# Optimization experiments

Hardware: AMD Instinct MI355X
Metric: run time of the kernel (lower is better)

## Reference

```python
import jax, jax.numpy as jnp
import numpy as np

B, T, D_IN, H, NUM_CLASSES = 1024, 512, 4, 64, 3
G = 4 * H  # gates: i, f, g, o (PyTorch order)


def setup_inputs() -> dict:
    key = jax.random.key(0)
    ks = jax.random.split(key, 32)
    s = 0.1  # small init scale, like PyTorch's 1/sqrt(H) uniform
    inp = {"x": jax.random.normal(ks[0], (B, T, D_IN), jnp.float32)}
    i = 1
    for l in range(4):
        d = D_IN if l == 0 else H
        inp[f"w_ih_{l}"] = s * jax.random.normal(ks[i], (G, d), jnp.float32); i += 1
        inp[f"w_hh_{l}"] = s * jax.random.normal(ks[i], (G, H), jnp.float32); i += 1
        inp[f"b_ih_{l}"] = s * jax.random.normal(ks[i], (G,), jnp.float32); i += 1
        inp[f"b_hh_{l}"] = s * jax.random.normal(ks[i], (G,), jnp.float32); i += 1
    inp["fc1_w"] = s * jax.random.normal(ks[i], (H // 2, H), jnp.float32); i += 1
    inp["fc1_b"] = s * jax.random.normal(ks[i], (H // 2,), jnp.float32); i += 1
    inp["fc2_w"] = s * jax.random.normal(ks[i], (NUM_CLASSES, H // 2), jnp.float32); i += 1
    inp["fc2_b"] = s * jax.random.normal(ks[i], (NUM_CLASSES,), jnp.float32)
    return inp


def _lstm_layer(x, w_ih, w_hh, b_ih, b_hh):
    # x: [B, T, d_in] -> [B, T, H]; PyTorch gate order i, f, g, o.
    b, t, _ = x.shape
    # Precompute input contribution for all timesteps in one GEMM.
    pre = jnp.einsum('btd,gd->tbg', x, w_ih) + (b_ih + b_hh)  # [T, B, 4H]
    h0 = jnp.zeros((b, H), x.dtype)
    c0 = jnp.zeros((b, H), x.dtype)

    def step(carry, p):
        h, c = carry
        gates = p + h @ w_hh.T  # [B, 4H]
        i_g, f_g, g_g, o_g = jnp.split(gates, 4, axis=-1)
        i_g = jax.nn.sigmoid(i_g)
        f_g = jax.nn.sigmoid(f_g)
        g_g = jnp.tanh(g_g)
        o_g = jax.nn.sigmoid(o_g)
        c = f_g * c + i_g * g_g
        h = o_g * jnp.tanh(c)
        return (h, c), h

    _, hs = jax.lax.scan(step, (h0, c0), pre)  # hs: [T, B, H]
    return hs.transpose(1, 0, 2)


def reference(x,
              w_ih_0, w_hh_0, b_ih_0, b_hh_0,
              w_ih_1, w_hh_1, b_ih_1, b_hh_1,
              w_ih_2, w_hh_2, b_ih_2, b_hh_2,
              w_ih_3, w_hh_3, b_ih_3, b_hh_3,
              fc1_w, fc1_b, fc2_w, fc2_b):
    layers = [(w_ih_0, w_hh_0, b_ih_0, b_hh_0),
              (w_ih_1, w_hh_1, b_ih_1, b_hh_1),
              (w_ih_2, w_hh_2, b_ih_2, b_hh_2),
              (w_ih_3, w_hh_3, b_ih_3, b_hh_3)]
    h = x
    for (wi, wh, bi, bh) in layers:
        h = _lstm_layer(h, wi, wh, bi, bh)
    last = h[:, -1, :]                         # [B, H]
    z = jax.nn.relu(last @ fc1_w.T + fc1_b)    # [B, H//2]
    logits = z @ fc2_w.T + fc2_b               # [B, 3]
    return jax.nn.softmax(logits, axis=1)
```

## Files before the change

kernel.cpp:

```cpp
#include <hip/hip_runtime.h>


#define TLEN 512
#define NCH  64

typedef __bf16 bf16x8 __attribute__((ext_vector_type(8)));
typedef float  f32x4  __attribute__((ext_vector_type(4)));

struct Params {
  const float* x;
  const float* wih[4]; const float* whh[4];
  const float* bih[4]; const float* bhh[4];
  const float* fc1w; const float* fc1b;
  const float* fc2w; const float* fc2b;
  float* out;
};

__device__ __forceinline__ bf16x8 bfzero() {
  union { unsigned long long u[2]; bf16x8 v; } z; z.u[0] = 0ull; z.u[1] = 0ull; return z.v;
}
__device__ __forceinline__ float fast_sigmoid(float x) {
  return __builtin_amdgcn_rcpf(1.f + __expf(-x));
}
__device__ __forceinline__ float fast_tanh(float x) {
  float e = __expf(2.f * x);
  return 1.f - 2.f * __builtin_amdgcn_rcpf(e + 1.f);
}

__global__ __launch_bounds__(1024) void lstm_fused(Params p)
{
  const int chunk = blockIdx.x;
  const int b0   = chunk * 16;
  const int tid  = threadIdx.x;
  const int wave = tid >> 6;
  const int L    = wave >> 2;
  const int w    = wave & 3;
  const int lane = tid & 63;
  const int quad = lane >> 4;
  const int l15  = lane & 15;

  __shared__ __bf16 tiles[2][5][16 * 64];
  __shared__ float  s_fc1w[2048];
  __shared__ float  s_z[512];
  __shared__ float  s_fc1b[32];
  __shared__ float  s_fc2w[96];
  __shared__ float  s_fc2b[3];

  bf16x8 wf[4][4];
  float  bias[4];
  {
    const float* wih = p.wih[L];
    const float* whh = p.whh[L];
    const float* bih = p.bih[L];
    const float* bhh = p.bhh[L];
#pragma unroll
    for (int g = 0; g < 4; g++) {
      int n = g * 64 + w * 16 + l15;
      bias[g] = bih[n] + bhh[n];
      if (L == 0) {
        bf16x8 f = bfzero();
        if (quad == 0) {
#pragma unroll
          for (int j = 0; j < 4; j++) f[j] = (__bf16)wih[n * 4 + j];
        }
        wf[g][0] = f; wf[g][1] = bfzero();
      } else {
#pragma unroll
        for (int q = 0; q < 2; q++) {
          const float* s = wih + n * 64 + q * 32 + quad * 8;
          bf16x8 f;
#pragma unroll
          for (int j = 0; j < 8; j++) f[j] = (__bf16)s[j];
          wf[g][q] = f;
        }
      }
#pragma unroll
      for (int q = 0; q < 2; q++) {
        const float* s = whh + n * 64 + q * 32 + quad * 8;
        bf16x8 f;
#pragma unroll
        for (int j = 0; j < 8; j++) f[j] = (__bf16)s[j];
        wf[g][2 + q] = f;
      }
    }
  }

  {
    int* ti = (int*)tiles;
    for (int i = tid; i < 5120; i += 1024) ti[i] = 0;
  }
  float cst[4] = {0.f, 0.f, 0.f, 0.f};

  if (wave == 0 && quad == 0) {
    const float4 xv = *(const float4*)(p.x + ((size_t)(b0 + l15) * TLEN) * 4);
    __bf16 v[4] = {(__bf16)xv.x, (__bf16)xv.y, (__bf16)xv.z, (__bf16)xv.w};
    *(float2*)&tiles[0][0][l15 * 64 + (l15 & 7) * 8] = *(float2*)v;
  }
  __syncthreads();

  for (int s = 0; s < TLEN + 3; s++) {
    const int t  = s - L;
    const int pr = s & 1;
    const int pw = pr ^ 1;

    if ((unsigned)t < (unsigned)TLEN) {
      const __bf16* in  = tiles[pr][L];
      const __bf16* own = tiles[pr][L + 1];
      const int sg0 = quad ^ (l15 & 7);
      const int sg1 = (4 + quad) ^ (l15 & 7);
      bf16x8 xf0 = *(const bf16x8*)&in [l15 * 64 + sg0 * 8];
      bf16x8 xf1 = *(const bf16x8*)&in [l15 * 64 + sg1 * 8];
      bf16x8 hf0 = *(const bf16x8*)&own[l15 * 64 + sg0 * 8];
      bf16x8 hf1 = *(const bf16x8*)&own[l15 * 64 + sg1 * 8];

      f32x4 acc[4];
#pragma unroll
      for (int g = 0; g < 4; g++) { f32x4 a = {bias[g], bias[g], bias[g], bias[g]}; acc[g] = a; }
#pragma unroll
      for (int g = 0; g < 4; g++) {
        acc[g] = __builtin_amdgcn_mfma_f32_16x16x32_bf16(xf0, wf[g][0], acc[g], 0, 0, 0);
        acc[g] = __builtin_amdgcn_mfma_f32_16x16x32_bf16(xf1, wf[g][1], acc[g], 0, 0, 0);
        acc[g] = __builtin_amdgcn_mfma_f32_16x16x32_bf16(hf0, wf[g][2], acc[g], 0, 0, 0);
        acc[g] = __builtin_amdgcn_mfma_f32_16x16x32_bf16(hf1, wf[g][3], acc[g], 0, 0, 0);
      }

      if (wave == 0 && quad == 0 && t + 1 < TLEN) {
        const float4 xv = *(const float4*)(p.x + ((size_t)(b0 + l15) * TLEN + (t + 1)) * 4);
        __bf16 v[4] = {(__bf16)xv.x, (__bf16)xv.y, (__bf16)xv.z, (__bf16)xv.w};
        *(float2*)&tiles[pw][0][l15 * 64 + (l15 & 7) * 8] = *(float2*)v;
      }

      const int col = w * 16 + l15;
      __bf16* dst = tiles[pw][L + 1];
#pragma unroll
      for (int r = 0; r < 4; r++) {
        float ig = fast_sigmoid(acc[0][r]);
        float fg = fast_sigmoid(acc[1][r]);
        float gg = fast_tanh(acc[2][r]);
        float og = fast_sigmoid(acc[3][r]);
        float c = fg * cst[r] + ig * gg;
        cst[r] = c;
        float h = og * fast_tanh(c);
        int m  = quad * 4 + r;
        int sg = (col >> 3) ^ (m & 7);
        dst[m * 64 + sg * 8 + (col & 7)] = (__bf16)h;
      }
    }

    __syncthreads();
  }

  for (int i = tid; i < 2048; i += 1024) s_fc1w[i] = p.fc1w[i];
  if (tid < 32) s_fc1b[tid] = p.fc1b[tid];
  if (tid < 96) s_fc2w[tid] = p.fc2w[tid];
  if (tid < 3)  s_fc2b[tid] = p.fc2b[tid];
  __syncthreads();
  if (tid < 512) {
    int m = tid >> 5, u = tid & 31;
    float sacc = s_fc1b[u];
    const float* wrow = &s_fc1w[u * 64];
    const __bf16* hfin = tiles[1][4];
#pragma unroll
    for (int k = 0; k < 64; k++) {
      int sg = (k >> 3) ^ (m & 7);
      sacc += (float)hfin[m * 64 + sg * 8 + (k & 7)] * wrow[k];
    }
    s_z[m * 32 + u] = fmaxf(sacc, 0.f);
  }
  __syncthreads();
  if (tid < 16) {
    int m = tid;
    float lg[3];
#pragma unroll
    for (int v = 0; v < 3; v++) {
      float sv = s_fc2b[v];
#pragma unroll
      for (int u = 0; u < 32; u++) sv += s_z[m * 32 + u] * s_fc2w[v * 32 + u];
      lg[v] = sv;
    }
    float mx = fmaxf(lg[0], fmaxf(lg[1], lg[2]));
    float e0 = __expf(lg[0] - mx), e1 = __expf(lg[1] - mx), e2 = __expf(lg[2] - mx);
    float inv = 1.f / (e0 + e1 + e2);
    float* o = p.out + (size_t)(b0 + m) * 3;
    o[0] = e0 * inv; o[1] = e1 * inv; o[2] = e2 * inv;
  }
}

extern "C" void kernel_launch(void* const* d_in, const int* in_sizes, int n_in,
                              void* d_out, int out_size, void* d_ws, size_t ws_size,
                              hipStream_t stream)
{
  (void)in_sizes; (void)n_in; (void)out_size; (void)d_ws; (void)ws_size;
  Params p;
  p.x = (const float*)d_in[0];
  for (int l = 0; l < 4; l++) {
    p.wih[l] = (const float*)d_in[1 + 4 * l];
    p.whh[l] = (const float*)d_in[2 + 4 * l];
    p.bih[l] = (const float*)d_in[3 + 4 * l];
    p.bhh[l] = (const float*)d_in[4 + 4 * l];
  }
  p.fc1w = (const float*)d_in[17];
  p.fc1b = (const float*)d_in[18];
  p.fc2w = (const float*)d_in[19];
  p.fc2b = (const float*)d_in[20];
  p.out = (float*)d_out;

  hipLaunchKernelGGL(lstm_fused, dim3(NCH), dim3(1024), 0, stream, p);
}
```

Before: 924.2 us.

## Split LSTM layers across two workgroups per chunk with a global-memory ring handoff

Adds a new kernel that runs layers 0-1 and layers 2-3 of each batch chunk in separate 512-thread workgroups (128 blocks total). The first workgroup streams its layer-1 hidden states to the second through a ring buffer in workspace memory, coordinated by atomic flag and ack counters with spin-waits. This spreads the work over twice as many CUs and shortens each block's pipeline skew and barrier cost. In exchange it adds cross-CU synchronisation latency on every step and needs both blocks of a chunk to be co-resident, otherwise the spin loops run until their cap. The old fused kernel remains as a fallback when the workspace is too small.

```diff
diff --git a/kernel.cpp b/kernel.cpp
--- a/kernel.cpp
+++ b/kernel.cpp
@@ -3,6 +3,8 @@
 
 #define TLEN 512
 #define NCH  64
+#define AG   __HIP_MEMORY_SCOPE_AGENT
+#define SPIN_CAP 500000
 
 typedef __bf16 bf16x8 __attribute__((ext_vector_type(8)));
 typedef float  f32x4  __attribute__((ext_vector_type(4)));
@@ -13,7 +15,8 @@
   const float* bih[4]; const float* bhh[4];
   const float* fc1w; const float* fc1b;
   const float* fc2w; const float* fc2b;
-  float* out;
+  float* out; char* ws;
+  int R; int Rmask; int D;
 };
 
 __device__ __forceinline__ bf16x8 bfzero() {
@@ -25,6 +28,279 @@
 __device__ __forceinline__ float fast_tanh(float x) {
   float e = __expf(2.f * x);
   return 1.f - 2.f * __builtin_amdgcn_rcpf(e + 1.f);
+}
+__device__ __forceinline__ void load_frag_pair(const unsigned short* sb, int l15, int quad,
+                                               bf16x8& f0, bf16x8& f1) {
+  const unsigned long long* a = (const unsigned long long*)(sb + l15 * 64 + quad * 8);
+  const unsigned long long* b = (const unsigned long long*)(sb + l15 * 64 + 32 + quad * 8);
+  union { bf16x8 v; unsigned long long u[2]; } c0, c1;
+  c0.u[0] = __hip_atomic_load(&a[0], __ATOMIC_RELAXED, AG);
+  c0.u[1] = __hip_atomic_load(&a[1], __ATOMIC_RELAXED, AG);
+  c1.u[0] = __hip_atomic_load(&b[0], __ATOMIC_RELAXED, AG);
+  c1.u[1] = __hip_atomic_load(&b[1], __ATOMIC_RELAXED, AG);
+  f0 = c0.v; f1 = c1.v;
+}
+
+__global__ __launch_bounds__(512, 2) void lstm_split(Params p)
+{
+  const int bid   = blockIdx.x;
+  const int role  = bid >> 6;
+  const int chunk = bid & 63;
+  const int b0    = chunk * 16;
+  const int tid   = threadIdx.x;
+  const int wave  = tid >> 6;
+  const int grp   = wave >> 2;
+  const int w     = wave & 3;
+  const int lane  = tid & 63;
+  const int quad  = lane >> 4;
+  const int l15   = lane & 15;
+  const int L     = role * 2 + grp;
+
+  __shared__ __bf16 tiles[2][2][1024];
+  __shared__ float  s_fc1w[2048];
+  __shared__ float  s_z[512];
+  __shared__ float  s_fc1b[32];
+  __shared__ float  s_fc2w[96];
+  __shared__ float  s_fc2b[3];
+
+  int* flagp = (int*)p.ws + chunk * 16;
+  int* ackp  = (int*)(p.ws + 16 * 1024) + chunk * 16;
+  unsigned short* ringc = (unsigned short*)(p.ws + 32 * 1024) + (size_t)chunk * p.R * 1024;
+  const int RM = p.Rmask;
+
+  bf16x8 wf[4][4];
+  float  bias[4];
+  {
+    const float* wih = p.wih[L];
+    const float* whh = p.whh[L];
+    const float* bih = p.bih[L];
+    const float* bhh = p.bhh[L];
+#pragma unroll
+    for (int g = 0; g < 4; g++) {
+      int n = g * 64 + w * 16 + l15;
+      bias[g] = bih[n] + bhh[n];
+      if (L == 0) {
+        bf16x8 f = bfzero();
+        if (quad == 0) {
+#pragma unroll
+          for (int j = 0; j < 4; j++) f[j] = (__bf16)wih[n * 4 + j];
+        }
+        wf[g][0] = f; wf[g][1] = bfzero();
+      } else {
+#pragma unroll
+        for (int q = 0; q < 2; q++) {
+          const float* s = wih + n * 64 + q * 32 + quad * 8;
+          bf16x8 f;
+#pragma unroll
+          for (int j = 0; j < 8; j++) f[j] = (__bf16)s[j];
+          wf[g][q] = f;
+        }
+      }
+#pragma unroll
+      for (int q = 0; q < 2; q++) {
+        const float* s = whh + n * 64 + q * 32 + quad * 8;
+        bf16x8 f;
+#pragma unroll
+        for (int j = 0; j < 8; j++) f[j] = (__bf16)s[j];
+        wf[g][2 + q] = f;
+      }
+    }
+  }
+
+  { int* ti = (int*)tiles; for (int i = tid; i < 2048; i += 512) ti[i] = 0; }
+  float cst[4] = {0.f, 0.f, 0.f, 0.f};
+
+  int W = 0, f_pend = 0;
+  int ackW = -1000000000, a_pend = -1000000000;
+  bf16x8 xA0 = bfzero(), xA1 = bfzero();
+
+  if (role == 0) {
+    if (grp == 0 && quad == 0) {
+      const float4 xv = *(const float4*)(p.x + ((size_t)(b0 + l15) * TLEN) * 4);
+      bf16x8 f = bfzero();
+      f[0] = (__bf16)xv.x; f[1] = (__bf16)xv.y; f[2] = (__bf16)xv.z; f[3] = (__bf16)xv.w;
+      xA0 = f;
+    }
+  } else if (grp == 0) {
+    const int G = (p.D > 2) ? p.D : 2;
+    int v = 0, it = 0;
+    do {
+      if (lane == 0) v = __hip_atomic_load(flagp, __ATOMIC_ACQUIRE, AG);
+      v = __shfl(v, 0);
+      if (v >= G) break;
+      __builtin_amdgcn_s_sleep(2);
+    } while (++it < SPIN_CAP);
+    W = v;
+    load_frag_pair(ringc, l15, quad, xA0, xA1);
+  }
+  __syncthreads();
+
+  for (int s = 0; s < TLEN + 1; s++) {
+    const int t  = s - grp;
+    const int pr = s & 1, pw = pr ^ 1;
+    bf16x8 xN0 = xA0, xN1 = xA1;
+
+    if ((unsigned)t < (unsigned)TLEN) {
+      bf16x8 if0, if1;
+      if (grp == 0) { if0 = xA0; if1 = xA1; }
+      else {
+        const __bf16* src = tiles[pr][0];
+        int sg0 = quad ^ (l15 & 7);
+        int sg1 = (4 + quad) ^ (l15 & 7);
+        if0 = *(const bf16x8*)&src[l15 * 64 + sg0 * 8];
+        if1 = *(const bf16x8*)&src[l15 * 64 + sg1 * 8];
+      }
+      bf16x8 hf0, hf1;
+      {
+        const __bf16* src = tiles[pr][grp];
+        int sg0 = quad ^ (l15 & 7);
+        int sg1 = (4 + quad) ^ (l15 & 7);
+        hf0 = *(const bf16x8*)&src[l15 * 64 + sg0 * 8];
+        hf1 = *(const bf16x8*)&src[l15 * 64 + sg1 * 8];
+      }
+
+      f32x4 acc[4];
+#pragma unroll
+      for (int g = 0; g < 4; g++) { f32x4 a = {bias[g], bias[g], bias[g], bias[g]}; acc[g] = a; }
+      if (L == 0) {
+#pragma unroll
+        for (int g = 0; g < 4; g++)
+          acc[g] = __builtin_amdgcn_mfma_f32_16x16x32_bf16(if0, wf[g][0], acc[g], 0, 0, 0);
+      } else {
+#pragma unroll
+        for (int g = 0; g < 4; g++) {
+          acc[g] = __builtin_amdgcn_mfma_f32_16x16x32_bf16(if0, wf[g][0], acc[g], 0, 0, 0);
+          acc[g] = __builtin_amdgcn_mfma_f32_16x16x32_bf16(if1, wf[g][1], acc[g], 0, 0, 0);
+        }
+      }
+#pragma unroll
+      for (int g = 0; g < 4; g++) {
+        acc[g] = __builtin_amdgcn_mfma_f32_16x16x32_bf16(hf0, wf[g][2], acc[g], 0, 0, 0);
+        acc[g] = __builtin_amdgcn_mfma_f32_16x16x32_bf16(hf1, wf[g][3], acc[g], 0, 0, 0);
+      }
+
+      if (role == 0 && grp == 0 && quad == 0 && t + 1 < TLEN) {
+        const float4 xv = *(const float4*)(p.x + ((size_t)(b0 + l15) * TLEN + (t + 1)) * 4);
+        bf16x8 f = bfzero();
+        f[0] = (__bf16)xv.x; f[1] = (__bf16)xv.y; f[2] = (__bf16)xv.z; f[3] = (__bf16)xv.w;
+        xN0 = f;
+      }
+      if (role == 0 && grp == 1 && t >= p.R && ackW < t + 1 - p.R) {
+        int v = ackW, it = 0;
+        do {
+          if (lane == 0) v = __hip_atomic_load(ackp, __ATOMIC_ACQUIRE, AG);
+          v = __shfl(v, 0);
+          if (v >= t + 1 - p.R) break;
+          __builtin_amdgcn_s_sleep(2);
+        } while (++it < SPIN_CAP);
+        ackW = v;
+      }
+
+      const int col = w * 16 + l15;
+      __bf16* dst = tiles[pw][grp];
+      unsigned hb[4];
+#pragma unroll
+      for (int r = 0; r < 4; r++) {
+        float ig = fast_sigmoid(acc[0][r]);
+        float fg = fast_sigmoid(acc[1][r]);
+        float gg = fast_tanh(acc[2][r]);
+        float og = fast_sigmoid(acc[3][r]);
+        float c = fg * cst[r] + ig * gg;
+        cst[r] = c;
+        float h = og * fast_tanh(c);
+        __bf16 hbf = (__bf16)h;
+        union { __bf16 b; unsigned short s; } cv; cv.b = hbf;
+        hb[r] = cv.s;
+        int m  = quad * 4 + r;
+        int sg = (col >> 3) ^ (m & 7);
+        dst[m * 64 + sg * 8 + (col & 7)] = hbf;
+      }
+      if (role == 0 && grp == 1) {
+        unsigned* rdst = (unsigned*)(ringc + (size_t)(t & RM) * 1024);
+#pragma unroll
+        for (int r = 0; r < 4; r++) {
+          unsigned v = hb[r];
+          unsigned o = (unsigned)__shfl_xor((int)v, 1);
+          if ((lane & 1) == 0) {
+            int m = quad * 4 + r;
+            __hip_atomic_store(&rdst[(m * 64 + col) >> 1], v | (o << 16), __ATOMIC_RELAXED, AG);
+          }
+        }
+      }
+    }
+
+    __syncthreads();
+
+    if (role == 0) {
+      if (tid == 0 && s >= 1)
+        __hip_atomic_store(flagp, s, __ATOMIC_RELAXED, AG);
+      if (grp == 1) {
+        int am = __shfl(a_pend, 0);
+        if (am > ackW) ackW = am;
+        if (lane == 0) a_pend = __hip_atomic_load(ackp, __ATOMIC_RELAXED, AG);
+      }
+    } else {
+      if (grp == 0) {
+        int fm = __shfl(f_pend, 0);
+        if (fm > W) W = fm;
+        if (lane == 0) f_pend = __hip_atomic_load(flagp, __ATOMIC_ACQUIRE, AG);
+        const int c = s;
+        if (c + 1 < TLEN) {
+          if (W < c + 2) {
+            int v = W, it = 0;
+            do {
+              if (lane == 0) v = __hip_atomic_load(flagp, __ATOMIC_ACQUIRE, AG);
+              v = __shfl(v, 0);
+              if (v >= c + 2) break;
+              __builtin_amdgcn_s_sleep(2);
+            } while (++it < SPIN_CAP);
+            W = v;
+          }
+          load_frag_pair(ringc + (size_t)((c + 1) & RM) * 1024, l15, quad, xN0, xN1);
+        }
+      }
+      if (tid == 0)
+        __hip_atomic_store(ackp, s, __ATOMIC_RELAXED, AG);
+    }
+    xA0 = xN0; xA1 = xN1;
+  }
+
+  if (role == 1) {
+    for (int i = tid; i < 2048; i += 512) s_fc1w[i] = p.fc1w[i];
+    if (tid < 32) s_fc1b[tid] = p.fc1b[tid];
+    if (tid < 96) s_fc2w[tid] = p.fc2w[tid];
+    if (tid < 3)  s_fc2b[tid] = p.fc2b[tid];
+    __syncthreads();
+    {
+      int m = tid >> 5, u = tid & 31;
+      float sacc = s_fc1b[u];
+      const float* wrow = &s_fc1w[u * 64];
+      const __bf16* hfin = tiles[1][1];
+#pragma unroll
+      for (int k = 0; k < 64; k++) {
+        int sg = (k >> 3) ^ (m & 7);
+        sacc += (float)hfin[m * 64 + sg * 8 + (k & 7)] * wrow[k];
+      }
+      s_z[m * 32 + u] = fmaxf(sacc, 0.f);
+    }
+    __syncthreads();
+    if (tid < 16) {
+      int m = tid;
+      float lg[3];
+#pragma unroll
+      for (int v = 0; v < 3; v++) {
+        float sv = s_fc2b[v];
+#pragma unroll
+        for (int u = 0; u < 32; u++) sv += s_z[m * 32 + u] * s_fc2w[v * 32 + u];
+        lg[v] = sv;
+      }
+      float mx = fmaxf(lg[0], fmaxf(lg[1], lg[2]));
+      float e0 = __expf(lg[0] - mx), e1 = __expf(lg[1] - mx), e2 = __expf(lg[2] - mx);
+      float inv = 1.f / (e0 + e1 + e2);
+      float* o = p.out + (size_t)(b0 + m) * 3;
+      o[0] = e0 * inv; o[1] = e1 * inv; o[2] = e2 * inv;
+    }
+  }
 }
 
 __global__ __launch_bounds__(1024) void lstm_fused(Params p)
@@ -85,10 +361,7 @@
     }
   }
 
-  {
-    int* ti = (int*)tiles;
-    for (int i = tid; i < 5120; i += 1024) ti[i] = 0;
-  }
+  { int* ti = (int*)tiles; for (int i = tid; i < 5120; i += 1024) ti[i] = 0; }
   float cst[4] = {0.f, 0.f, 0.f, 0.f};
 
   if (wave == 0 && quad == 0) {
@@ -146,7 +419,6 @@
         dst[m * 64 + sg * 8 + (col & 7)] = (__bf16)h;
       }
     }
-
     __syncthreads();
   }
 
@@ -190,7 +462,7 @@
                               void* d_out, int out_size, void* d_ws, size_t ws_size,
                               hipStream_t stream)
 {
-  (void)in_sizes; (void)n_in; (void)out_size; (void)d_ws; (void)ws_size;
+  (void)in_sizes; (void)n_in; (void)out_size;
   Params p;
   p.x = (const float*)d_in[0];
   for (int l = 0; l < 4; l++) {
@@ -204,6 +476,19 @@
   p.fc2w = (const float*)d_in[19];
   p.fc2b = (const float*)d_in[20];
   p.out = (float*)d_out;
-
-  hipLaunchKernelGGL(lstm_fused, dim3(NCH), dim3(1024), 0, stream, p);
-}
+  p.ws  = (char*)d_ws;
+
+  const size_t slotbytes = (size_t)NCH * 2048;
+  const size_t avail = (ws_size > 32768) ? (ws_size - 32768) : 0;
+  int R = 1;
+  while (R < 32 && (size_t)(R * 2) * slotbytes <= avail) R <<= 1;
+
+  if (R >= 8) {
+    p.R = R; p.Rmask = R - 1;
+    p.D = (R - 2 < 6) ? (R - 2) : 6;
+    hipLaunchKernelGGL(lstm_split, dim3(128), dim3(512), 0, stream, p);
+  } else {
+    p.R = 0; p.Rmask = 0; p.D = 0;
+    hipLaunchKernelGGL(lstm_fused, dim3(NCH), dim3(1024), 0, stream, p);
+  }
+}
```

After: 2.222 ms. +140.4%, slower.
